# Performance work log

Measured on AMD Instinct MI355X. Metric: run time of the kernel, lower is better.

The kernel has to match this reference:

```python
import jax, jax.numpy as jnp
import numpy as np

KERNEL = 10   # kernel_size (asserted == 10 in the original)
HEADS = 4
BN_SCALE = 1.0 / np.sqrt(1.0 + 1e-5)  # eval-mode BatchNorm1d (running mean 0, var 1, affine 1/0)


def get_dct_matrix(N):
    k = np.arange(N)[:, None].astype(np.float64)
    i = np.arange(N)[None, :].astype(np.float64)
    w = np.full((N, 1), np.sqrt(2.0 / N))
    w[0, 0] = np.sqrt(1.0 / N)
    dct_m = w * np.cos(np.pi * (i + 0.5) * k / N)
    idct_m = np.linalg.inv(dct_m)
    return dct_m.astype(np.float32), idct_m.astype(np.float32)


def conv1d(x, w):  # x [B,C,L], w [O,I,K], valid, no bias
    return jax.lax.conv_general_dilated(x, w, (1,), 'VALID',
                                        dimension_numbers=('NCH', 'OIH', 'NCH'))


def conv_stack(x, w1, w2):  # Conv1d(k=6) -> ReLU -> Conv1d(k=5) -> ReLU
    return jax.nn.relu(conv1d(jax.nn.relu(conv1d(x, w1)), w2))


# vmap over the 4 heads' weights -> [H,B,D,L]
heads_conv = jax.vmap(conv_stack, in_axes=(None, 0, 0))


def _forward(src, cq1, cq2, ck1, ck2, lw, lb, giw, gia, gib, gbw, gba, gbb,
             gow, goa, gob, dct_n, output_n, input_n):
    bs, in_feat = src.shape[0], src.shape[2]
    src = src[:, :input_n]                                   # [B,50,48]
    src_key = jnp.swapaxes(src, 1, 2)[:, :, :input_n - output_n]  # [B,48,25]
    src_query = jnp.swapaxes(src, 1, 2)[:, :, -KERNEL:]           # [B,48,10]

    dct_np, idct_np = get_dct_matrix(KERNEL + output_n)
    dct_m = jnp.asarray(dct_np)
    idct_m = jnp.asarray(idct_np)

    vn = input_n - KERNEL - output_n + 1  # 16 overlapping value windows
    vl = KERNEL + output_n                # window length 35
    idx = np.arange(vl)[None, :] + np.arange(vn)[:, None]    # [16,35]
    windows = src[:, idx]                                    # [B,16,35,48]
    # DCT per window then flatten per-joint coeffs: [B,16,48*dct_n]
    val = jnp.einsum('dv,bnvf->bndf', dct_m[:dct_n], windows)
    src_value = jnp.swapaxes(val, 2, 3).reshape(bs, vn, -1)  # [B,16,480]

    key_h = heads_conv(src_key / 1000.0, ck1, ck2)           # [H,B,512,16]
    query_h = heads_conv(src_query / 1000.0, cq1, cq2)       # [H,B,512,1]

    # sum-normalized (non-softmax) attention
    score = jnp.einsum('hbdq,hbdk->hbqk', query_h, key_h) + 1e-15  # [H,B,1,16]
    att_w = score / jnp.sum(score, axis=3, keepdims=True)
    dct_att = jnp.einsum('hbk,bkf->hbf', att_w[:, :, 0], src_value)  # [H,B,480]
    dct_att = dct_att.reshape(HEADS, bs, in_feat, dct_n)
    att_cat = jnp.transpose(dct_att, (1, 0, 2, 3)).reshape(bs, HEADS * in_feat, dct_n)
    # Linear over the concatenated head/joint axis: [B,48,dct_n]
    att_lin = jnp.einsum('bmd,nm->bnd', att_cat, lw) + lb[None, :, None]

    # last kernel_size frames + last frame repeated output_n times
    gather_idx = np.concatenate([np.arange(input_n - KERNEL, input_n),
                                 np.full(output_n, input_n - 1)])
    input_gcn = src[:, gather_idx]                           # [B,35,48]
    dct_in = jnp.einsum('dv,bvf->bfd', dct_m[:dct_n], input_gcn)  # [B,48,10]
    dct_in = jnp.concatenate([dct_in, att_lin], axis=-1)     # [B,48,20]

    # GCN (Mao et al. style): learnable adjacency [48,48], eval-mode BN, tanh
    def gc(h, a, w, b):
        return jnp.einsum('nm,bmf->bnf', a, h @ w) + b

    y = jnp.tanh(gc(dct_in, gia, giw, gib) * BN_SCALE)       # [B,48,512]
    for s in range(gbw.shape[0]):
        r = y
        for j in range(2):
            y = jnp.tanh(gc(y, gba[s, j], gbw[s, j], gbb[s, j]) * BN_SCALE)
        y = y + r
    dct_out = gc(y, goa, gow, gob) + dct_in                  # [B,48,20]

    out_gcn = jnp.einsum('vd,bnd->bvn', idct_m[:, :dct_n], dct_out[:, :, :dct_n])  # [B,35,48]
    return out_gcn[:, :, None, :]                            # [B,35,itera=1,48]


def setup_inputs() -> dict:
    key = jax.random.key(0)
    ks = jax.random.split(key, 16)
    bs, in_feat, d_model, dct_n = 256, 48, 512, 10
    s = 0.05
    return {
        'src': jax.random.normal(ks[0], (bs, 50, in_feat), jnp.float32) * 1000.0,
        'convQ_w1': jax.random.normal(ks[1], (HEADS, d_model, in_feat, 6), jnp.float32) * s,
        'convQ_w2': jax.random.normal(ks[2], (HEADS, d_model, d_model, 5), jnp.float32) * s,
        'convK_w1': jax.random.normal(ks[3], (HEADS, d_model, in_feat, 6), jnp.float32) * s,
        'convK_w2': jax.random.normal(ks[4], (HEADS, d_model, d_model, 5), jnp.float32) * s,
        'linear_w': jax.random.normal(ks[5], (in_feat, HEADS * in_feat), jnp.float32) * s,
        'linear_b': jax.random.normal(ks[6], (in_feat,), jnp.float32) * s,
        'gc_in_w': jax.random.normal(ks[7], (2 * dct_n, d_model), jnp.float32) * s,
        'gc_in_att': jax.random.normal(ks[8], (in_feat, in_feat), jnp.float32) * s,
        'gc_in_b': jax.random.normal(ks[9], (d_model,), jnp.float32) * s,
        'gcb_w': jax.random.normal(ks[10], (2, 2, d_model, d_model), jnp.float32) * s,
        'gcb_att': jax.random.normal(ks[11], (2, 2, in_feat, in_feat), jnp.float32) * s,
        'gcb_b': jax.random.normal(ks[12], (2, 2, d_model), jnp.float32) * s,
        'gc_out_w': jax.random.normal(ks[13], (d_model, 2 * dct_n), jnp.float32) * s,
        'gc_out_att': jax.random.normal(ks[14], (in_feat, in_feat), jnp.float32) * s,
        'gc_out_b': jax.random.normal(ks[15], (2 * dct_n,), jnp.float32) * s,
        'dct_n': 10, 'output_n': 25, 'input_n': 50, 'itera': 1,
    }


def reference(src, convQ_w1, convQ_w2, convK_w1, convK_w2, linear_w, linear_b,
              gc_in_w, gc_in_att, gc_in_b, gcb_w, gcb_att, gcb_b,
              gc_out_w, gc_out_att, gc_out_b, dct_n, output_n, input_n, itera):
    # itera=1 path only (itera>1 in the original references undefined attrs)
    return _forward(src, convQ_w1, convQ_w2, convK_w1, convK_w2, linear_w, linear_b,
                    gc_in_w, gc_in_att, gc_in_b, gcb_w, gcb_att, gcb_b,
                    gc_out_w, gc_out_att, gc_out_b, dct_n, output_n, input_n)
```

## Files before the change

### kernel.cpp

```cpp
#include <hip/hip_runtime.h>
#include <math.h>

static constexpr float BN_SCALE_F = 0.9999950000374997f;

typedef __bf16 bf16;
typedef bf16 bf16x8 __attribute__((ext_vector_type(8)));
typedef bf16 bf16x4 __attribute__((ext_vector_type(4)));
typedef float floatx4 __attribute__((ext_vector_type(4)));

#define GLOBAL_AS __attribute__((address_space(1)))
#define LDS_AS __attribute__((address_space(3)))

__device__ __forceinline__ float tanh_fast(float x) {
    const float e = __expf(2.f * x);
    return 1.f - 2.f / (e + 1.f);
}

__device__ __forceinline__ void d_trw1(int id, const float* w, bf16* wt) {
    if (id < 4 * 512 * 320) {
        int ho = id / 320, c = id % 320;
        float v = (c < 288) ? w[(long)ho * 288 + (c % 48) * 6 + (c / 48)] * 1e-3f : 0.f;
        wt[id] = (bf16)v;
    }
}
__global__ __launch_bounds__(256) void k_prep(
    const float* __restrict__ src, const float* __restrict__ cq1,
    const float* __restrict__ ck1, const float* __restrict__ cq2,
    const float* __restrict__ ck2, const float* __restrict__ gbw,
    const float* __restrict__ giw, const float* __restrict__ gow,
    const float* __restrict__ gba, float* __restrict__ dct10,
    bf16* __restrict__ srcbf, bf16* __restrict__ w1tq, bf16* __restrict__ w1tk,
    bf16* __restrict__ w2tq, bf16* __restrict__ w2tk, bf16* __restrict__ gbwF,
    bf16* __restrict__ giwF, bf16* __restrict__ gowT, bf16* __restrict__ gbaP) {
    __shared__ float lds[4160];
    int bb = blockIdx.x;
    const int t = threadIdx.x;
    if (bb < 2) {
        int id = bb * 256 + t;
        if (id < 350) {
            int k = id / 35, i = id % 35;
            double w = (k == 0) ? sqrt(1.0 / 35.0) : sqrt(2.0 / 35.0);
            dct10[id] = (float)(w * cos(3.14159265358979323846 * (i + 0.5) * k / 35.0));
        }
        return;
    }
    bb -= 2;
    if (bb < 2401) {
        int id = bb * 256 + t;
        if (id < 614656) srcbf[id] = (bf16)(id < 614400 ? src[id] : 0.f);
        return;
    }
    bb -= 2401;
    if (bb < 2560) { d_trw1(bb * 256 + t, cq1, w1tq); return; }
    bb -= 2560;
    if (bb < 2560) { d_trw1(bb * 256 + t, ck1, w1tk); return; }
    bb -= 2560;
    if (bb < 4096) {
        const bool isQ = bb < 2048;
        const int ho = isQ ? bb : bb - 2048;
        const float* wrow = (isQ ? cq2 : ck2) + (long)ho * 2560;
        bf16* orow = (isQ ? w2tq : w2tk) + (long)ho * 2560;
        for (int j = t; j < 2560; j += 256) lds[j] = wrow[j];
        __syncthreads();
        for (int c = t; c < 2560; c += 256) {
            const int k = c >> 9, ii = c & 511;
            orow[c] = (bf16)lds[ii * 5 + k];
        }
        return;
    }
    bb -= 4096;
    if (bb < 256) {
        const int l = bb >> 6, tile = bb & 63;
        const int tr = tile >> 3, tc = tile & 7;
        const float* in = gbw + (long)l * 262144;
        bf16* o = gbwF + (long)l * 262144;
#pragma unroll
        for (int r = 0; r < 16; ++r) {
            const int kl = (t >> 6) * 16 + r, ml = t & 63;
            lds[kl * 65 + ml] = in[(long)(tr * 64 + kl) * 512 + tc * 64 + ml];
        }
        __syncthreads();
        for (int j = t; j < 4096; j += 256) {
            const int q = j >> 9, r4 = j & 511;
            const int gl = q >> 2, sl = (q >> 1) & 1, jt = q & 1;
            const int lane = r4 >> 3, e = r4 & 7;
            const int fr = lane & 15, fq = lane >> 4;
            const int kk = sl * 32 + fq * 8 + e;
            const int ff = gl * 32 + jt * 16 + fr;
            o[(long)(tc * 2 + gl) * 16384 + (long)(tr * 2 + sl) * 1024 + jt * 512 + r4] =
                (bf16)lds[kk * 65 + ff];
        }
        return;
    }
    bb -= 256;
    if (bb < 128) {
        int id = bb * 256 + t;
        if (id < 32768) {
            const int r2 = id & 2047;
            const int s = r2 >> 10, r3 = r2 & 1023;
            const int jt = r3 >> 9, r4 = r3 & 511;
            const int lane = r4 >> 3, e = r4 & 7;
            const int fr = lane & 15, fq = lane >> 4;
            const int g = id >> 11;
            const int k = s * 32 + fq * 8 + e;
            const int f = g * 32 + jt * 16 + fr;
            giwF[id] = (bf16)(k < 20 ? giw[k * 512 + f] : 0.f);
        }
        return;
    }
    bb -= 128;
    if (bb < 64) {
        int id = bb * 256 + t;
        int d = id >> 9, k = id & 511;
        gowT[id] = (bf16)(d < 20 ? gow[k * 20 + d] : 0.f);
        return;
    }
    bb -= 64;
    {
        int id = bb * 256 + t;
        if (id < 12288) {
            int l = id / 3072, r = id % 3072, n = r >> 6, m = r & 63;
            gbaP[id] = (bf16)(m < 48 ? gba[l * 2304 + n * 48 + m] : 0.f);
        }
    }
}

__global__ __launch_bounds__(256) void k_conv1(
    const bf16* __restrict__ w1tk, const bf16* __restrict__ w1tq,
    const bf16* __restrict__ srcbf, bf16* __restrict__ r1k,
    bf16* __restrict__ r1q) {
    int bx, by, bz;
    const bf16* A;
    bf16* C;
    int NT, toff;
    long cStr;
    {
        const int i = blockIdx.x;
        if (i < 1280) {
            bz = i / 320;
            const int r = i % 320;
            bx = r % 40;
            by = r / 40;
            A = w1tk; C = r1k; NT = 20; toff = 0; cStr = 2621440L;
        } else {
            const int j = i - 1280;
            bz = j / 80;
            const int r = j % 80;
            bx = r % 10;
            by = r / 10;
            A = w1tq; C = r1q; NT = 5; toff = 40; cStr = 655360L;
        }
    }
    __shared__ bf16 As[64 * 64];
    __shared__ bf16 Bs[128 * 64];
    const int tid = threadIdx.x;
    const int wave = tid >> 6;
    const int lane = tid & 63;
    const int wm = (wave & 1) * 32;
    const int wn = (wave >> 1) * 64;
    const int m0 = by * 64;
    const int n0 = bx * 128;
    A += (long)bz * (512L * 320);

    const int srow = lane >> 3;
    const int gch = (lane & 7) ^ srow;
    const bf16* aptr[2];
    const bf16* bptr[4];
#pragma unroll
    for (int i = 0; i < 2; ++i) {
        const int ar = wave * 16 + i * 8 + srow;
        aptr[i] = A + (long)(m0 + ar) * 320 + gch * 8;
    }
#pragma unroll
    for (int i = 0; i < 4; ++i) {
        const int ar = wave * 32 + i * 8 + srow;
        const int n = n0 + ar;
        const long bbase = (long)(n / NT) * 2400 + (long)((n % NT) + toff) * 48;
        bptr[i] = srcbf + bbase + gch * 8;
    }

    floatx4 acc[4][2];
#pragma unroll
    for (int j = 0; j < 4; ++j)
#pragma unroll
        for (int i = 0; i < 2; ++i) acc[j][i] = (floatx4){0.f, 0.f, 0.f, 0.f};

    const int fr = lane & 15;
    const int fq = lane >> 4;
    const int fx = lane & 7;

    for (int k0 = 0; k0 < 320; k0 += 64) {
#pragma unroll
        for (int i = 0; i < 2; ++i)
            __builtin_amdgcn_global_load_lds(
                (const GLOBAL_AS void*)(aptr[i] + k0),
                (LDS_AS void*)(As + (wave * 16 + i * 8) * 64), 16, 0, 0);
#pragma unroll
        for (int i = 0; i < 4; ++i)
            __builtin_amdgcn_global_load_lds(
                (const GLOBAL_AS void*)(bptr[i] + k0),
                (LDS_AS void*)(Bs + (wave * 32 + i * 8) * 64), 16, 0, 0);
        __syncthreads();
#pragma unroll
        for (int kk = 0; kk < 2; ++kk) {
            bf16x8 af[2], bfr[4];
#pragma unroll
            for (int im = 0; im < 2; ++im)
                af[im] = *(const bf16x8*)(As + (wm + im * 16 + fr) * 64 +
                                          ((((kk << 2) + fq) ^ fx) << 3));
#pragma unroll
            for (int in = 0; in < 4; ++in)
                bfr[in] = *(const bf16x8*)(Bs + (wn + in * 16 + fr) * 64 +
                                           ((((kk << 2) + fq) ^ fx) << 3));
#pragma unroll
            for (int in = 0; in < 4; ++in)
#pragma unroll
                for (int im = 0; im < 2; ++im)
                    acc[in][im] = __builtin_amdgcn_mfma_f32_16x16x32_bf16(
                        af[im], bfr[in], acc[in][im], 0, 0, 0);
        }
        __syncthreads();
    }
#pragma unroll
    for (int in = 0; in < 4; ++in) {
        const long n = n0 + wn + in * 16 + fr;
#pragma unroll
        for (int im = 0; im < 2; ++im) {
            floatx4 v = acc[in][im];
            const long m = m0 + wm + im * 16 + (fq << 2);
            v.x = fmaxf(v.x, 0.f);
            v.y = fmaxf(v.y, 0.f);
            v.z = fmaxf(v.z, 0.f);
            v.w = fmaxf(v.w, 0.f);
            bf16* Cp = C + (long)bz * cStr + n * 512 + m;
            bf16x4 ov;
            ov[0] = (bf16)v.x;
            ov[1] = (bf16)v.y;
            ov[2] = (bf16)v.z;
            ov[3] = (bf16)v.w;
            *(bf16x4*)Cp = ov;
        }
    }
}

__global__ __launch_bounds__(256) void k_conv2(
    const bf16* __restrict__ w2tk, const bf16* __restrict__ r1k,
    bf16* __restrict__ keyh, const bf16* __restrict__ w2tq,
    const bf16* __restrict__ r1q, bf16* __restrict__ qh) {
    const int K = 2560;
    int bx, by, bz;
    const bf16 *A, *B;
    bf16* C;
    bool r1kMode;
    long aStr, bStr, cStr;
    {
        const int i = blockIdx.x;
        if (i < 1024) {
            const int slot = i & 7;
            bz = slot >> 1;
            const int half = slot & 1;
            const int j = i >> 3;
            bx = half * 16 + (j & 15);
            by = j >> 4;
            A = w2tk; B = r1k; C = keyh; r1kMode = true;
            aStr = 512L * 2560; bStr = 2621440L; cStr = 2097152L;
        } else {
            const int j = i - 1024;
            bz = j >> 4;
            const int r = j & 15;
            bx = r & 1;
            by = r >> 1;
            A = w2tq; B = r1q; C = qh; r1kMode = false;
            aStr = 512L * 2560; bStr = 655360L; cStr = 131072L;
        }
    }
    __shared__ bf16 As[64 * 64];
    __shared__ bf16 Bs[128 * 64];
    const int tid = threadIdx.x;
    const int wave = tid >> 6;
    const int lane = tid & 63;
    const int wm = (wave & 1) * 32;
    const int wn = (wave >> 1) * 64;
    const int m0 = by * 64;
    const int n0 = bx * 128;
    A += (long)bz * aStr;
    B += (long)bz * bStr;

    const int srow = lane >> 3;
    const int gch = (lane & 7) ^ srow;
    const bf16* aptr[2];
    const bf16* bptr[4];
#pragma unroll
    for (int i = 0; i < 2; ++i) {
        const int ar = wave * 16 + i * 8 + srow;
        aptr[i] = A + (long)(m0 + ar) * K + gch * 8;
    }
#pragma unroll
    for (int i = 0; i < 4; ++i) {
        const int ar = wave * 32 + i * 8 + srow;
        const int n = n0 + ar;
        const long bbase = r1kMode ? (long)((n >> 4) * 20 + (n & 15)) * 512
                                   : (long)n * K;
        bptr[i] = B + bbase + gch * 8;
    }

    floatx4 acc[4][2];
#pragma unroll
    for (int j = 0; j < 4; ++j)
#pragma unroll
        for (int i = 0; i < 2; ++i) acc[j][i] = (floatx4){0.f, 0.f, 0.f, 0.f};

    const int fr = lane & 15;
    const int fq = lane >> 4;
    const int fx = lane & 7;

    for (int k0 = 0; k0 < K; k0 += 64) {
#pragma unroll
        for (int i = 0; i < 2; ++i)
            __builtin_amdgcn_global_load_lds(
                (const GLOBAL_AS void*)(aptr[i] + k0),
                (LDS_AS void*)(As + (wave * 16 + i * 8) * 64), 16, 0, 0);
#pragma unroll
        for (int i = 0; i < 4; ++i)
            __builtin_amdgcn_global_load_lds(
                (const GLOBAL_AS void*)(bptr[i] + k0),
                (LDS_AS void*)(Bs + (wave * 32 + i * 8) * 64), 16, 0, 0);
        __syncthreads();
#pragma unroll
        for (int kk = 0; kk < 2; ++kk) {
            bf16x8 af[2], bfr[4];
#pragma unroll
            for (int im = 0; im < 2; ++im)
                af[im] = *(const bf16x8*)(As + (wm + im * 16 + fr) * 64 +
                                          ((((kk << 2) + fq) ^ fx) << 3));
#pragma unroll
            for (int in = 0; in < 4; ++in)
                bfr[in] = *(const bf16x8*)(Bs + (wn + in * 16 + fr) * 64 +
                                           ((((kk << 2) + fq) ^ fx) << 3));
#pragma unroll
            for (int in = 0; in < 4; ++in)
#pragma unroll
                for (int im = 0; im < 2; ++im)
                    acc[in][im] = __builtin_amdgcn_mfma_f32_16x16x32_bf16(
                        af[im], bfr[in], acc[in][im], 0, 0, 0);
        }
        __syncthreads();
    }
#pragma unroll
    for (int in = 0; in < 4; ++in) {
        const long n = n0 + wn + in * 16 + fr;
#pragma unroll
        for (int im = 0; im < 2; ++im) {
            floatx4 v = acc[in][im];
            const long m = m0 + wm + im * 16 + (fq << 2);
            v.x = fmaxf(v.x, 0.f);
            v.y = fmaxf(v.y, 0.f);
            v.z = fmaxf(v.z, 0.f);
            v.w = fmaxf(v.w, 0.f);
            bf16* Cp = C + (long)bz * cStr + n * 512 + m;
            bf16x4 ov;
            ov[0] = (bf16)v.x;
            ov[1] = (bf16)v.y;
            ov[2] = (bf16)v.z;
            ov[3] = (bf16)v.w;
            *(bf16x4*)Cp = ov;
        }
    }
}

__global__ __launch_bounds__(512) void k_att(
    const bf16* __restrict__ qh, const bf16* __restrict__ keyh,
    const float* __restrict__ src, const float* __restrict__ dct10,
    const float* __restrict__ lw, const float* __restrict__ lb,
    const float* __restrict__ gia, float* __restrict__ dctin,
    bf16* __restrict__ z0) {
    const int b = blockIdx.x;
    const int t = threadIdx.x;
    __shared__ float BIG[9216];
    __shared__ float WD[2400];
    __shared__ float D[350];
    __shared__ float L[1920];
    __shared__ float dinS[960];
    __shared__ float sS[64];
    __shared__ float awS[64];

    {
        const int g = t >> 3, lane = t & 7;
        const int h = g >> 4, tt = g & 15;
        const bf16* q = qh + ((long)h * 256 + b) * 512 + lane * 64;
        const bf16* kr = keyh + (long)h * 2097152 + ((long)b * 16 + tt) * 512 + lane * 64;
        float p = 0.f;
#pragma unroll
        for (int i = 0; i < 8; ++i) {
            const bf16x8 qv = *(const bf16x8*)(q + i * 8);
            const bf16x8 kv = *(const bf16x8*)(kr + i * 8);
#pragma unroll
            for (int j = 0; j < 8; ++j) p = fmaf((float)qv[j], (float)kv[j], p);
        }
        p += __shfl_down(p, 4, 8);
        p += __shfl_down(p, 2, 8);
        p += __shfl_down(p, 1, 8);
        if (lane == 0) sS[g] = p + 1e-15f;
    }
    for (int i = t; i < 2400; i += 512) WD[i] = src[(long)b * 2400 + i];
    for (int i = t; i < 350; i += 512) D[i] = dct10[i];
    __syncthreads();
    if (t < 4) {
        float s = 0.f;
#pragma unroll
        for (int k = 0; k < 16; ++k) s += sS[t * 16 + k];
        const float inv = 1.f / s;
#pragma unroll
        for (int k = 0; k < 16; ++k) awS[t * 16 + k] = sS[t * 16 + k] * inv;
    }
    __syncthreads();
    if (t < 480) {
        const int f = t / 10, d = t % 10;
        float dreg[35];
#pragma unroll
        for (int v = 0; v < 35; ++v) dreg[v] = D[d * 35 + v];
#pragma unroll 2
        for (int n = 0; n < 16; ++n) {
            float acc = 0.f;
#pragma unroll
            for (int v = 0; v < 35; ++v)
                acc = fmaf(dreg[v], WD[(n + v) * 48 + f], acc);
            BIG[n * 480 + t] = acc;
        }
        float acc = 0.f;
#pragma unroll
        for (int v = 0; v < 10; ++v)
            acc = fmaf(dreg[v], WD[(40 + v) * 48 + f], acc);
        float cs = 0.f;
#pragma unroll
        for (int v = 10; v < 35; ++v) cs += dreg[v];
        acc = fmaf(cs, WD[49 * 48 + f], acc);
        dinS[f * 20 + d] = acc;
        dctin[(long)b * 960 + f * 20 + d] = acc;
    }
    __syncthreads();
    for (int p = 0; p < 4; ++p) {
        const int idx = t + p * 512;
        if (idx < 1920) {
            const int h = idx / 480, j = idx % 480;
            float acc = 0.f;
#pragma unroll
            for (int k = 0; k < 16; ++k)
                acc = fmaf(awS[h * 16 + k], BIG[k * 480 + j], acc);
            L[idx] = acc;
        }
    }
    __syncthreads();
    for (int i = t; i < 9216; i += 512) BIG[i] = lw[i];
    for (int i = t; i < 2304; i += 512) WD[i] = gia[i];
    __syncthreads();
    if (t < 480) {
        const int n = t / 10, d = t % 10;
        float acc = lb[n];
#pragma unroll
        for (int h = 0; h < 4; ++h)
#pragma unroll
            for (int f = 0; f < 48; ++f)
                acc = fmaf(BIG[n * 192 + h * 48 + f], L[h * 480 + f * 10 + d], acc);
        dinS[n * 20 + 10 + d] = acc;
        dctin[(long)b * 960 + n * 20 + 10 + d] = acc;
    }
    __syncthreads();
    for (int p = 0; p < 2; ++p) {
        const int idx = t + p * 512;
        if (idx < 960) {
            const int n = idx / 20, d = idx % 20;
            float acc = 0.f;
#pragma unroll
            for (int m = 0; m < 48; ++m)
                acc = fmaf(WD[n * 48 + m], dinS[m * 20 + d], acc);
            z0[((long)b * 48 + n) * 64 + d] = (bf16)acc;
        }
    }
    for (int i = t; i < 2112; i += 512) {
        const int n = i / 44, c = 20 + i % 44;
        z0[((long)b * 48 + n) * 64 + c] = (bf16)0.f;
    }
}

template <bool TOUT, int S>
__device__ __forceinline__ void gcn_matmul3(
    const bf16* __restrict__ zSrc, const bf16* __restrict__ Wf,
    const float* __restrict__ bias, const bf16* __restrict__ resT,
    bf16* __restrict__ outS, const int wave, const int lane) {
    const int fr = lane & 15, fq = lane >> 4;
    const int f0 = wave * 32;
    floatx4 acc[3][2];
#pragma unroll
    for (int it = 0; it < 3; ++it)
#pragma unroll
        for (int jt = 0; jt < 2; ++jt) acc[it][jt] = (floatx4){0.f, 0.f, 0.f, 0.f};
    const bf16* wp = Wf + (long)wave * (S * 1024) + (lane << 3);
    bf16x8 w0[4], w1[4];
    constexpr int PRE = (S < 3) ? S : 3;
#pragma unroll
    for (int s = 0; s < PRE; ++s) {
        w0[s] = *(const bf16x8*)(wp + s * 1024);
        w1[s] = *(const bf16x8*)(wp + s * 1024 + 512);
    }
#pragma unroll
    for (int s = 0; s < S; ++s) {
        bf16x8 af[3];
#pragma unroll
        for (int it = 0; it < 3; ++it)
            af[it] = *(const bf16x8*)(zSrc + (it * 16 + fr) * 520 + s * 32 + fq * 8);
        if (s + 3 < S) {
            const int ns = (s + 3) & 3;
            w0[ns] = *(const bf16x8*)(wp + (s + 3) * 1024);
            w1[ns] = *(const bf16x8*)(wp + (s + 3) * 1024 + 512);
        }
        const int sl = s & 3;
#pragma unroll
        for (int it = 0; it < 3; ++it) {
            acc[it][0] = __builtin_amdgcn_mfma_f32_16x16x32_bf16(af[it], w0[sl],
                                                                acc[it][0], 0, 0, 0);
            acc[it][1] = __builtin_amdgcn_mfma_f32_16x16x32_bf16(af[it], w1[sl],
                                                                acc[it][1], 0, 0, 0);
        }
    }
#pragma unroll
    for (int jt = 0; jt < 2; ++jt) {
        const int f = f0 + jt * 16 + fr;
        const float bv = bias[f];
#pragma unroll
        for (int it = 0; it < 3; ++it) {
            const int ir0 = it * 16 + fq * 4;
            float v[4];
#pragma unroll
            for (int r = 0; r < 4; ++r)
                v[r] = tanh_fast((acc[it][jt][r] + bv) * BN_SCALE_F);
            if (resT) {
                const bf16x4 rv = *(const bf16x4*)(resT + f * 48 + ir0);
#pragma unroll
                for (int r = 0; r < 4; ++r) v[r] += (float)rv[r];
            }
            if (TOUT) {
                bf16x4 ov;
#pragma unroll
                for (int r = 0; r < 4; ++r) ov[r] = (bf16)v[r];
                *(bf16x4*)(outS + f * 48 + ir0) = ov;
            } else {
#pragma unroll
                for (int r = 0; r < 4; ++r)
                    outS[(ir0 + r) * 520 + f] = (bf16)v[r];
            }
        }
    }
}

__device__ __forceinline__ void gcn_attmul2(const bf16* __restrict__ gA,
                                            const bf16* __restrict__ YinT,
                                            bf16* __restrict__ zOut,
                                            const int wave, const int lane) {
    const int fr = lane & 15, fq = lane >> 4;
    const int f0 = wave * 32;
    floatx4 acc[3][2];
#pragma unroll
    for (int it = 0; it < 3; ++it)
#pragma unroll
        for (int jt = 0; jt < 2; ++jt) acc[it][jt] = (floatx4){0.f, 0.f, 0.f, 0.f};
    bf16x8 af0[3], af1[3], bv0[2], bv1[2];
#pragma unroll
    for (int it = 0; it < 3; ++it) {
        af0[it] = *(const bf16x8*)(gA + (it * 16 + fr) * 64 + fq * 8);
        af1[it] = *(const bf16x8*)(gA + (it * 16 + fr) * 64 + 32 + fq * 8);
    }
#pragma unroll
    for (int jt = 0; jt < 2; ++jt) {
        const int f = f0 + jt * 16 + fr;
        bv0[jt] = *(const bf16x8*)(YinT + f * 48 + fq * 8);
        bv1[jt] = *(const bf16x8*)(YinT + f * 48 + 32 + fq * 8);
    }
#pragma unroll
    for (int it = 0; it < 3; ++it)
#pragma unroll
        for (int jt = 0; jt < 2; ++jt) {
            acc[it][jt] = __builtin_amdgcn_mfma_f32_16x16x32_bf16(af0[it], bv0[jt],
                                                                 acc[it][jt], 0, 0, 0);
            acc[it][jt] = __builtin_amdgcn_mfma_f32_16x16x32_bf16(af1[it], bv1[jt],
                                                                 acc[it][jt], 0, 0, 0);
        }
#pragma unroll
    for (int jt = 0; jt < 2; ++jt) {
        const int f = f0 + jt * 16 + fr;
#pragma unroll
        for (int it = 0; it < 3; ++it)
#pragma unroll
            for (int r = 0; r < 4; ++r)
                zOut[(it * 16 + fq * 4 + r) * 520 + f] = (bf16)acc[it][jt][r];
    }
}

__global__ __launch_bounds__(1024) void k_gcn(
    const bf16* __restrict__ z0, const bf16* __restrict__ giwF,
    const float* __restrict__ gib, const bf16* __restrict__ gbwF,
    const bf16* __restrict__ gbaP, const float* __restrict__ gbb,
    const float* __restrict__ goa, const bf16* __restrict__ gowT,
    const float* __restrict__ gob, const float* __restrict__ dctin,
    const float* __restrict__ dct10, float* __restrict__ out) {
    const int b = blockIdx.x;
    const int t = threadIdx.x;
    const int wave = t >> 6, lane = t & 63;
    __shared__ __align__(16) bf16 yaS[24976];
    __shared__ __align__(16) bf16 ybS[24592];
    __shared__ __align__(16) bf16 zS[48 * 520];

    if (t < 384) {
        const int r = t >> 3, c = t & 7;
        *(bf16x8*)(zS + r * 520 + c * 8) =
            *(const bf16x8*)(z0 + ((long)b * 48 + r) * 64 + c * 8);
    } else if (t < 400) {
        yaS[24576 + (t - 384)] = (bf16)0.f;
    } else if (t < 416) {
        ybS[24576 + (t - 400)] = (bf16)0.f;
    }
    __syncthreads();
    gcn_matmul3<true, 2>(zS, giwF, gib, nullptr, yaS, wave, lane);
    __syncthreads();

#pragma unroll
    for (int l = 0; l < 4; ++l) {
        const bf16* YinT = (l == 0 || l == 3) ? yaS : ybS;
        gcn_attmul2(gbaP + l * 3072, YinT, zS, wave, lane);
        __syncthreads();
        const bf16* Res = (l == 1) ? yaS : (l == 3 ? ybS : nullptr);
        if (l < 3)
            gcn_matmul3<true, 16>(zS, gbwF + (long)l * 262144, gbb + l * 512,
                                  Res, (l < 2) ? ybS : yaS, wave, lane);
        else
            gcn_matmul3<false, 16>(zS, gbwF + 3L * 262144, gbb + 3 * 512, Res,
                                   yaS, wave, lane);
        __syncthreads();
    }
    float* T2 = (float*)ybS;
    float* dS = ((float*)ybS) + 960;
    float* goaS = ((float*)ybS) + 1920;
    float* Df = ((float*)ybS) + 4224;
    if (t < 384) {
        const int fr2 = lane & 15, fq2 = lane >> 4;
        const int it = wave >> 1, jt = wave & 1;
        floatx4 accT = (floatx4){0.f, 0.f, 0.f, 0.f};
        const bf16* ap = yaS + (it * 16 + fr2) * 520 + fq2 * 8;
        const bf16* gp = gowT + (long)(jt * 16 + fr2) * 512 + fq2 * 8;
        for (int k0 = 0; k0 < 512; k0 += 32) {
            const bf16x8 av = *(const bf16x8*)(ap + k0);
            const bf16x8 gv = *(const bf16x8*)(gp + k0);
            accT = __builtin_amdgcn_mfma_f32_16x16x32_bf16(av, gv, accT, 0, 0, 0);
        }
        const int d = jt * 16 + fr2;
        if (d < 20) {
#pragma unroll
            for (int r = 0; r < 4; ++r) {
                const int m = it * 16 + fq2 * 4 + r;
                T2[m * 20 + d] = accT[r];
            }
        }
    } else {
        for (int i = t - 384; i < 2304; i += 640) goaS[i] = goa[i];
        for (int i = t - 384; i < 350; i += 640) Df[i] = dct10[i];
    }
    __syncthreads();
    if (t < 960) {
        const int n = t / 20, d = t % 20;
        float acc = gob[d] + dctin[(long)b * 960 + t];
#pragma unroll
        for (int m = 0; m < 48; ++m)
            acc = fmaf(goaS[n * 48 + m], T2[m * 20 + d], acc);
        dS[t] = acc;
    }
    __syncthreads();
    for (int e = t; e < 1680; e += 1024) {
        const int v = e / 48, n = e % 48;
        float acc = 0.f;
#pragma unroll
        for (int d = 0; d < 10; ++d)
            acc = fmaf(Df[d * 35 + v], dS[n * 20 + d], acc);
        out[(long)b * 1680 + e] = acc;
    }
}

static constexpr size_t WS_DCT10 = 0;
static constexpr size_t WS_ATTW = 1536;
static constexpr size_t WS_QH = WS_ATTW + 65536;
static constexpr size_t WS_DCTIN = WS_QH + 2097152;
static constexpr size_t WS_DCTOUT = WS_DCTIN + 983040;
static constexpr size_t WS_SRCVAL = WS_DCTOUT + 983040;
static constexpr size_t WS_PAD0 = WS_SRCVAL + 7864320;
static constexpr size_t WS_GOWT = WS_PAD0;
static constexpr size_t WS_GBAP = WS_PAD0 + 32768;
static constexpr size_t WS_SRCBF = WS_PAD0 + 8388608;
static constexpr size_t WS_W1TQ = WS_SRCBF + 1229824;
static constexpr size_t WS_W1TK = WS_W1TQ + 1310720;
static constexpr size_t WS_W2TQ = WS_W1TK + 1310720;
static constexpr size_t WS_W2TK = WS_W2TQ + 10485760;
static constexpr size_t WS_GBWT = WS_W2TK + 10485760;
static constexpr size_t WS_R1K = WS_GBWT + 2097152;
static constexpr size_t WS_R1Q = WS_R1K + 20971520;
static constexpr size_t WS_T = WS_R1Q + 5242880;
static constexpr size_t WS_GIWP = WS_T + 50331648;
static constexpr size_t WS_KEYH = WS_T;
static constexpr size_t WS_Z0 = WS_T + 17825792;

extern "C" void kernel_launch(void* const* d_in, const int* in_sizes, int n_in,
                              void* d_out, int out_size, void* d_ws,
                              size_t ws_size, hipStream_t stream) {
    const float* src = (const float*)d_in[0];
    const float* cq1 = (const float*)d_in[1];
    const float* cq2 = (const float*)d_in[2];
    const float* ck1 = (const float*)d_in[3];
    const float* ck2 = (const float*)d_in[4];
    const float* lw = (const float*)d_in[5];
    const float* lb = (const float*)d_in[6];
    const float* giw = (const float*)d_in[7];
    const float* gia = (const float*)d_in[8];
    const float* gib = (const float*)d_in[9];
    const float* gbw = (const float*)d_in[10];
    const float* gba = (const float*)d_in[11];
    const float* gbb = (const float*)d_in[12];
    const float* gow = (const float*)d_in[13];
    const float* goa = (const float*)d_in[14];
    const float* gob = (const float*)d_in[15];
    float* out = (float*)d_out;
    char* ws = (char*)d_ws;

    float* dct10 = (float*)(ws + WS_DCT10);
    bf16* qh = (bf16*)(ws + WS_QH);
    float* dctin = (float*)(ws + WS_DCTIN);
    bf16* keyh = (bf16*)(ws + WS_KEYH);
    bf16* srcbf = (bf16*)(ws + WS_SRCBF);
    bf16* w1tq = (bf16*)(ws + WS_W1TQ);
    bf16* w1tk = (bf16*)(ws + WS_W1TK);
    bf16* w2tq = (bf16*)(ws + WS_W2TQ);
    bf16* w2tk = (bf16*)(ws + WS_W2TK);
    bf16* gbwF = (bf16*)(ws + WS_GBWT);
    bf16* r1k = (bf16*)(ws + WS_R1K);
    bf16* r1q = (bf16*)(ws + WS_R1Q);
    bf16* giwF = (bf16*)(ws + WS_GIWP);
    bf16* gowT = (bf16*)(ws + WS_GOWT);
    bf16* gbaP = (bf16*)(ws + WS_GBAP);
    bf16* z0 = (bf16*)(ws + WS_Z0);

    k_prep<<<12115, 256, 0, stream>>>(src, cq1, ck1, cq2, ck2, gbw, giw, gow,
                                      gba, dct10, srcbf, w1tq, w1tk, w2tq,
                                      w2tk, gbwF, giwF, gowT, gbaP);

    k_conv1<<<1600, 256, 0, stream>>>(w1tk, w1tq, srcbf, r1k, r1q);

    k_conv2<<<1088, 256, 0, stream>>>(w2tk, r1k, keyh, w2tq, r1q, qh);

    k_att<<<256, 512, 0, stream>>>(qh, keyh, src, dct10, lw, lb, gia, dctin, z0);

    k_gcn<<<256, 1024, 0, stream>>>(z0, giwF, gib, gbwF, gbaP, gbb, goa, gowT,
                                    gob, dctin, dct10, out);
}
```

Measured before the change: 302.7 us.

## Reuse conv1 output rows across the five conv2 taps in key GEMM

```diff
diff --git a/kernel.cpp b/kernel.cpp
--- a/kernel.cpp
+++ b/kernel.cpp
@@ -251,7 +251,7 @@
     int bx, by, bz;
     const bf16 *A, *B;
     bf16* C;
-    bool r1kMode;
+    bool kMode;
     long aStr, bStr, cStr;
     {
         const int i = blockIdx.x;
@@ -262,7 +262,7 @@
             const int j = i >> 3;
             bx = half * 16 + (j & 15);
             by = j >> 4;
-            A = w2tk; B = r1k; C = keyh; r1kMode = true;
+            A = w2tk; B = r1k; C = keyh; kMode = true;
             aStr = 512L * 2560; bStr = 2621440L; cStr = 2097152L;
         } else {
             const int j = i - 1024;
@@ -270,12 +270,12 @@
             const int r = j & 15;
             bx = r & 1;
             by = r >> 1;
-            A = w2tq; B = r1q; C = qh; r1kMode = false;
+            A = w2tq; B = r1q; C = qh; kMode = false;
             aStr = 512L * 2560; bStr = 655360L; cStr = 131072L;
         }
     }
     __shared__ bf16 As[64 * 64];
-    __shared__ bf16 Bs[128 * 64];
+    __shared__ bf16 Bs[160 * 64];
     const int tid = threadIdx.x;
     const int wave = tid >> 6;
     const int lane = tid & 63;
@@ -289,20 +289,11 @@
     const int srow = lane >> 3;
     const int gch = (lane & 7) ^ srow;
     const bf16* aptr[2];
-    const bf16* bptr[4];
 #pragma unroll
     for (int i = 0; i < 2; ++i) {
         const int ar = wave * 16 + i * 8 + srow;
         aptr[i] = A + (long)(m0 + ar) * K + gch * 8;
     }
-#pragma unroll
-    for (int i = 0; i < 4; ++i) {
-        const int ar = wave * 32 + i * 8 + srow;
-        const int n = n0 + ar;
-        const long bbase = r1kMode ? (long)((n >> 4) * 20 + (n & 15)) * 512
-                                   : (long)n * K;
-        bptr[i] = B + bbase + gch * 8;
-    }
 
     floatx4 acc[4][2];
 #pragma unroll
@@ -314,37 +305,99 @@
     const int fq = lane >> 4;
     const int fx = lane & 7;
 
-    for (int k0 = 0; k0 < K; k0 += 64) {
-#pragma unroll
-        for (int i = 0; i < 2; ++i)
-            __builtin_amdgcn_global_load_lds(
-                (const GLOBAL_AS void*)(aptr[i] + k0),
-                (LDS_AS void*)(As + (wave * 16 + i * 8) * 64), 16, 0, 0);
-#pragma unroll
-        for (int i = 0; i < 4; ++i)
-            __builtin_amdgcn_global_load_lds(
-                (const GLOBAL_AS void*)(bptr[i] + k0),
-                (LDS_AS void*)(Bs + (wave * 32 + i * 8) * 64), 16, 0, 0);
-        __syncthreads();
-#pragma unroll
-        for (int kk = 0; kk < 2; ++kk) {
-            bf16x8 af[2], bfr[4];
-#pragma unroll
-            for (int im = 0; im < 2; ++im)
-                af[im] = *(const bf16x8*)(As + (wm + im * 16 + fr) * 64 +
-                                          ((((kk << 2) + fq) ^ fx) << 3));
-#pragma unroll
-            for (int in = 0; in < 4; ++in)
-                bfr[in] = *(const bf16x8*)(Bs + (wn + in * 16 + fr) * 64 +
-                                           ((((kk << 2) + fq) ^ fx) << 3));
-#pragma unroll
-            for (int in = 0; in < 4; ++in)
+    if (kMode) {
+        const bf16* bptrK[5];
+        int ldsBK[5];
+#pragma unroll
+        for (int j = 0; j < 5; ++j) {
+            const int rloc = wave * 40 + j * 8 + srow;
+            const int brel = rloc / 20, pos = rloc % 20;
+            bptrK[j] = B + ((long)((bx * 8 + brel) * 20 + pos)) * 512 +
+                       ((lane & 7) ^ (pos & 7)) * 8;
+            ldsBK[j] = rloc * 64 + (lane & 7) * 8;
+        }
+        const int bq = wn >> 4;
+        for (int c0i = 0; c0i < 8; ++c0i) {
+            const int c0 = c0i * 64;
+#pragma unroll
+            for (int w = 0; w < 5; ++w) {
+                const int k0 = w * 512 + c0;
+#pragma unroll
+                for (int i = 0; i < 2; ++i)
+                    __builtin_amdgcn_global_load_lds(
+                        (const GLOBAL_AS void*)(aptr[i] + k0),
+                        (LDS_AS void*)(As + (wave * 16 + i * 8) * 64), 16, 0, 0);
+                if (w == 0) {
+#pragma unroll
+                    for (int j = 0; j < 5; ++j)
+                        __builtin_amdgcn_global_load_lds(
+                            (const GLOBAL_AS void*)(bptrK[j] + c0),
+                            (LDS_AS void*)(Bs + ldsBK[j]), 16, 0, 0);
+                }
+                __syncthreads();
+#pragma unroll
+                for (int kk = 0; kk < 2; ++kk) {
+                    bf16x8 af[2], bfr[4];
+#pragma unroll
+                    for (int im = 0; im < 2; ++im)
+                        af[im] = *(const bf16x8*)(As + (wm + im * 16 + fr) * 64 +
+                                                  ((((kk << 2) + fq) ^ fx) << 3));
+#pragma unroll
+                    for (int nt = 0; nt < 4; ++nt) {
+                        const int row = (bq + nt) * 20 + fr + w;
+                        bfr[nt] = *(const bf16x8*)(
+                            Bs + row * 64 +
+                            ((((kk << 2) + fq) ^ ((fr + w) & 7)) << 3));
+                    }
+#pragma unroll
+                    for (int nt = 0; nt < 4; ++nt)
+#pragma unroll
+                        for (int im = 0; im < 2; ++im)
+                            acc[nt][im] = __builtin_amdgcn_mfma_f32_16x16x32_bf16(
+                                af[im], bfr[nt], acc[nt][im], 0, 0, 0);
+                }
+                __syncthreads();
+            }
+        }
+    } else {
+        const bf16* bptr[4];
+#pragma unroll
+        for (int i = 0; i < 4; ++i) {
+            const int ar = wave * 32 + i * 8 + srow;
+            bptr[i] = B + (long)(n0 + ar) * K + gch * 8;
+        }
+        for (int k0 = 0; k0 < K; k0 += 64) {
+#pragma unroll
+            for (int i = 0; i < 2; ++i)
+                __builtin_amdgcn_global_load_lds(
+                    (const GLOBAL_AS void*)(aptr[i] + k0),
+                    (LDS_AS void*)(As + (wave * 16 + i * 8) * 64), 16, 0, 0);
+#pragma unroll
+            for (int i = 0; i < 4; ++i)
+                __builtin_amdgcn_global_load_lds(
+                    (const GLOBAL_AS void*)(bptr[i] + k0),
+                    (LDS_AS void*)(Bs + (wave * 32 + i * 8) * 64), 16, 0, 0);
+            __syncthreads();
+#pragma unroll
+            for (int kk = 0; kk < 2; ++kk) {
+                bf16x8 af[2], bfr[4];
 #pragma unroll
                 for (int im = 0; im < 2; ++im)
-                    acc[in][im] = __builtin_amdgcn_mfma_f32_16x16x32_bf16(
-                        af[im], bfr[in], acc[in][im], 0, 0, 0);
-        }
-        __syncthreads();
+                    af[im] = *(const bf16x8*)(As + (wm + im * 16 + fr) * 64 +
+                                              ((((kk << 2) + fq) ^ fx) << 3));
+#pragma unroll
+                for (int in = 0; in < 4; ++in)
+                    bfr[in] = *(const bf16x8*)(Bs + (wn + in * 16 + fr) * 64 +
+                                               ((((kk << 2) + fq) ^ fx) << 3));
+#pragma unroll
+                for (int in = 0; in < 4; ++in)
+#pragma unroll
+                    for (int im = 0; im < 2; ++im)
+                        acc[in][im] = __builtin_amdgcn_mfma_f32_16x16x32_bf16(
+                            af[im], bfr[in], acc[in][im], 0, 0, 0);
+            }
+            __syncthreads();
+        }
     }
 #pragma unroll
     for (int in = 0; in < 4; ++in) {
```

Result: no change. 302.9 us (median of 2 runs) (+0.1%).
